# Performance work log

Measured on AMD Instinct MI355X. Metric: run time of the kernel, lower is better.

The kernel has to match this reference:

```python
import jax, jax.numpy as jnp
import numpy as np

S, B, K = 64, 16, 512
QD, KD, A = 512, 512, 256


def setup_inputs() -> dict:
    key = jax.random.key(0)
    ks = jax.random.split(key, 10)
    inv_q = 1.0 / np.sqrt(QD)
    inv_k = 1.0 / np.sqrt(KD)
    inv_a = 1.0 / np.sqrt(A)
    return {
        "queries": jax.random.normal(ks[0], (S, B, QD), dtype=jnp.float32),
        "keys": jax.random.normal(ks[1], (B, K, KD), dtype=jnp.float32),
        "null_mask": jax.random.randint(ks[2], (B, K), 0, 2).astype(jnp.bool_),
        # nn.Linear params (PyTorch layout: weight (out, in), bias (out,))
        "Ww": jax.random.uniform(ks[3], (A, QD), jnp.float32, -inv_q, inv_q),
        "Wb": jax.random.uniform(ks[4], (A,), jnp.float32, -inv_q, inv_q),
        "Uw": jax.random.uniform(ks[5], (A, KD), jnp.float32, -inv_k, inv_k),
        "Ub": jax.random.uniform(ks[6], (A,), jnp.float32, -inv_k, inv_k),
        "vw": jax.random.uniform(ks[7], (1, A), jnp.float32, -inv_a, inv_a),
        "vb": jax.random.uniform(ks[8], (1,), jnp.float32, -inv_a, inv_a),
    }


def reference(queries, keys, null_mask, Ww, Wb, Uw, Ub, vw, vb):
    # t_query: (S, B, A); t_key: (B, K, A)
    t_query = jnp.einsum("sbq,aq->sba", queries, Ww) + Wb
    t_key = jnp.einsum("bkd,ad->bka", keys, Uw) + Ub
    # broadcast add -> (S, B, K, A), tanh, project with v -> alpha (S, B, K)
    h = jnp.tanh(t_query[:, :, None, :] + t_key[None, :, :, :])
    alpha = jnp.einsum("sbka,a->sbk", h, vw[0]) + vb[0]
    alpha = jnp.where(null_mask[None, :, :], -jnp.inf, alpha)
    att_weight = jax.nn.softmax(alpha, axis=2)  # (S, B, K)
    # bmm(att_weight^T, keys)^T -> (S, B, KD)
    attened_keys = jnp.einsum("sbk,bkd->sbd", att_weight, keys)
    return attened_keys, alpha
```

## Files before the change

### kernel.cpp

```cpp
#include <hip/hip_runtime.h>
#include <math.h>

#define S_DIM 64
#define B_DIM 16
#define K_DIM 512
#define QD_DIM 512
#define A_DIM 256

#define NEG_BIG (-3.0e38f)

#define SC 2.8853900817779268f

#define TK_OFF 262144
#define W_WS_OFF ((size_t)2359296)
#define CONV_F32_OFF ((size_t)2883584)
#define CONV_ROWS 9728
#define LO_USHORT_OFF ((size_t)CONV_ROWS * 512)

typedef __attribute__((ext_vector_type(8))) short short8v;
typedef __attribute__((ext_vector_type(4))) float f32x4;

static __device__ __forceinline__ uint2 pack_hi4(float4 v) {
    unsigned x0 = __float_as_uint(v.x), x1 = __float_as_uint(v.y),
             x2 = __float_as_uint(v.z), x3 = __float_as_uint(v.w);
    uint2 r;
    r.x = (x1 & 0xffff0000u) | (x0 >> 16);
    r.y = (x3 & 0xffff0000u) | (x2 >> 16);
    return r;
}
static __device__ __forceinline__ uint2 pack_lo4(float4 v) {
    float l0 = v.x - __uint_as_float(__float_as_uint(v.x) & 0xffff0000u);
    float l1 = v.y - __uint_as_float(__float_as_uint(v.y) & 0xffff0000u);
    float l2 = v.z - __uint_as_float(__float_as_uint(v.z) & 0xffff0000u);
    float l3 = v.w - __uint_as_float(__float_as_uint(v.w) & 0xffff0000u);
    unsigned y0 = __float_as_uint(l0), y1 = __float_as_uint(l1),
             y2 = __float_as_uint(l2), y3 = __float_as_uint(l3);
    uint2 r;
    r.x = (y1 & 0xffff0000u) | (y0 >> 16);
    r.y = (y3 & 0xffff0000u) | (y2 >> 16);
    return r;
}

__global__ __launch_bounds__(256) void conv_kernel(
    const float* __restrict__ q, const float* __restrict__ k,
    const float* __restrict__ ww, const float* __restrict__ uw,
    unsigned short* __restrict__ hi, unsigned short* __restrict__ lo)
{
    const int idx = blockIdx.x * 256 + threadIdx.x;
    const int row = idx >> 6;
    const int c   = (idx & 63) << 3;

    const float* __restrict__ src;
    if (row < 1024)      src = q  + (size_t)row * 512;
    else if (row < 9216) src = k  + (size_t)(row - 1024) * 512;
    else if (row < 9472) src = ww + (size_t)(row - 9216) * 512;
    else                 src = uw + (size_t)(row - 9472) * 512;

    float4 v0 = *(const float4*)(src + c);
    float4 v1 = *(const float4*)(src + c + 4);
    uint2 h0 = pack_hi4(v0), h1 = pack_hi4(v1);
    uint2 l0 = pack_lo4(v0), l1 = pack_lo4(v1);
    uint4 H = {h0.x, h0.y, h1.x, h1.y};
    uint4 L = {l0.x, l0.y, l1.x, l1.y};
    *(uint4*)&hi[(size_t)row * 512 + c] = H;
    *(uint4*)&lo[(size_t)row * 512 + c] = L;
}

__global__ __launch_bounds__(256) void lin_mfma(
    const unsigned short* __restrict__ hi, const unsigned short* __restrict__ lo,
    const float* __restrict__ Wb, const float* __restrict__ Ub,
    float* __restrict__ t_ws)
{
    __shared__ unsigned short Ah[64][40], Al[64][40], Bh[64][40], Bl[64][40];

    const int bx = blockIdx.x;
    const bool isQ = (bx < 64);
    int mt, nt;
    if (isQ) { mt = bx >> 2; nt = bx & 3; }
    else     { int t = bx - 64; mt = t >> 7; nt = t & 127; }

    const int aro = isQ ? (mt * 64) : (9472 + mt * 64);
    const int bro = isQ ? (9216 + nt * 64) : (1024 + nt * 64);

    const int tid  = threadIdx.x;
    const int srow = tid >> 2;
    const int scol = (tid & 3) << 3;
    const int lane = tid & 63, wid = tid >> 6;
    const int wm = (wid >> 1) << 5, wn = (wid & 1) << 5;
    const int fr  = lane & 15;
    const int fkb = (lane >> 4) << 3;

    f32x4 acc[2][2] = {};

    const unsigned short* pAh = hi + (size_t)(aro + srow) * 512 + scol;
    const unsigned short* pAl = lo + (size_t)(aro + srow) * 512 + scol;
    const unsigned short* pBh = hi + (size_t)(bro + srow) * 512 + scol;
    const unsigned short* pBl = lo + (size_t)(bro + srow) * 512 + scol;

    uint4 rah = *(const uint4*)(pAh);
    uint4 ral = *(const uint4*)(pAl);
    uint4 rbh = *(const uint4*)(pBh);
    uint4 rbl = *(const uint4*)(pBl);

    for (int ks = 0; ks < 16; ++ks) {
        __syncthreads();
        *(uint4*)&Ah[srow][scol] = rah;
        *(uint4*)&Al[srow][scol] = ral;
        *(uint4*)&Bh[srow][scol] = rbh;
        *(uint4*)&Bl[srow][scol] = rbl;
        __syncthreads();
        if (ks < 15) {
            const int o = (ks + 1) * 32;
            rah = *(const uint4*)(pAh + o);
            ral = *(const uint4*)(pAl + o);
            rbh = *(const uint4*)(pBh + o);
            rbl = *(const uint4*)(pBl + o);
        }
        short8v bhv[2], blv[2];
        #pragma unroll
        for (int j = 0; j < 2; ++j) {
            bhv[j] = *(const short8v*)&Bh[wn + j * 16 + fr][fkb];
            blv[j] = *(const short8v*)&Bl[wn + j * 16 + fr][fkb];
        }
        #pragma unroll
        for (int i = 0; i < 2; ++i) {
            short8v ah = *(const short8v*)&Ah[wm + i * 16 + fr][fkb];
            short8v al = *(const short8v*)&Al[wm + i * 16 + fr][fkb];
            #pragma unroll
            for (int j = 0; j < 2; ++j) {
                acc[i][j] = __builtin_amdgcn_mfma_f32_16x16x32_bf16(ah, bhv[j], acc[i][j], 0, 0, 0);
                acc[i][j] = __builtin_amdgcn_mfma_f32_16x16x32_bf16(ah, blv[j], acc[i][j], 0, 0, 0);
                acc[i][j] = __builtin_amdgcn_mfma_f32_16x16x32_bf16(al, bhv[j], acc[i][j], 0, 0, 0);
            }
        }
    }

    const int crow = (lane >> 4) << 2;
    if (isQ) {
        #pragma unroll
        for (int j = 0; j < 2; ++j) {
            const int a_col = nt * 64 + wn + j * 16 + fr;
            const float bias = Wb[a_col];
            #pragma unroll
            for (int i = 0; i < 2; ++i)
                #pragma unroll
                for (int r = 0; r < 4; ++r) {
                    const int m = mt * 64 + wm + i * 16 + crow + r;
                    t_ws[(size_t)m * 256 + a_col] =
                        __builtin_amdgcn_exp2f(SC * (acc[i][j][r] + bias));
                }
        }
    } else {
        #pragma unroll
        for (int i = 0; i < 2; ++i)
            #pragma unroll
            for (int r = 0; r < 4; ++r) {
                const int a = mt * 64 + wm + i * 16 + crow + r;
                const float bias = Ub[a];
                #pragma unroll
                for (int j = 0; j < 2; ++j) {
                    const int n = nt * 64 + wn + j * 16 + fr;
                    t_ws[TK_OFF + (size_t)(n >> 9) * 131072 + (size_t)a * 512 + (n & 511)]
                        = __builtin_amdgcn_exp2f(SC * (acc[i][j][r] + bias));
                }
            }
    }
}

__global__ __launch_bounds__(256) void alpha_kernel(
    const float* __restrict__ t_ws, const float* __restrict__ vw,
    const float* __restrict__ vb, const unsigned char* __restrict__ mask,
    float* __restrict__ alpha_out, float* __restrict__ w_ws)
{
    __shared__ float4 pv[256];
    __shared__ float red[5][4];

    const int bid = blockIdx.x;
    const int b  = bid >> 5;
    const int sp = (bid & 31) << 1;
    const int tid = threadIdx.x;
    const int lane = tid & 63, wid = tid >> 6;

    const float myvw = vw[tid];
    {
        float4 p;
        p.x = t_ws[(size_t)(sp * B_DIM + b) * A_DIM + tid];
        p.y = t_ws[(size_t)((sp + 1) * B_DIM + b) * A_DIM + tid];
        p.z = myvw; p.w = 0.f;
        pv[tid] = p;
    }

    float sv = myvw;
    #pragma unroll
    for (int o = 32; o > 0; o >>= 1) sv += __shfl_xor(sv, o);
    if (lane == 0) red[0][wid] = sv;
    __syncthreads();
    const float sumvw = red[0][0] + red[0][1] + red[0][2] + red[0][3];

    const float* __restrict__ ek = t_ws + TK_OFF + (size_t)b * 131072;
    const int k2 = tid * 2;

    float acc00 = 0.f, acc01 = 0.f, acc10 = 0.f, acc11 = 0.f;
    #pragma unroll 4
    for (int a = 0; a < A_DIM; ++a) {
        float2 tv = *(const float2*)&ek[(size_t)a * 512 + k2];
        float4 p = pv[a];
        float r00 = __builtin_amdgcn_rcpf(fmaf(p.x, tv.x, 1.0f));
        float r01 = __builtin_amdgcn_rcpf(fmaf(p.x, tv.y, 1.0f));
        float r10 = __builtin_amdgcn_rcpf(fmaf(p.y, tv.x, 1.0f));
        float r11 = __builtin_amdgcn_rcpf(fmaf(p.y, tv.y, 1.0f));
        acc00 = fmaf(p.z, r00, acc00);
        acc01 = fmaf(p.z, r01, acc01);
        acc10 = fmaf(p.z, r10, acc10);
        acc11 = fmaf(p.z, r11, acc11);
    }

    const float base = sumvw + vb[0];
    float a00 = base - 2.0f * acc00, a01 = base - 2.0f * acc01;
    float a10 = base - 2.0f * acc10, a11 = base - 2.0f * acc11;
    const unsigned char* mrow = mask + b * K_DIM;
    const bool m0 = mrow[k2] != 0, m1 = mrow[k2 + 1] != 0;
    if (m0) { a00 = NEG_BIG; a10 = NEG_BIG; }
    if (m1) { a01 = NEG_BIG; a11 = NEG_BIG; }

    *(float2*)&alpha_out[(size_t)(sp * B_DIM + b) * K_DIM + k2] = make_float2(a00, a01);
    *(float2*)&alpha_out[(size_t)((sp + 1) * B_DIM + b) * K_DIM + k2] = make_float2(a10, a11);

    float mm0 = fmaxf(a00, a01), mm1 = fmaxf(a10, a11);
    #pragma unroll
    for (int o = 32; o > 0; o >>= 1) {
        mm0 = fmaxf(mm0, __shfl_xor(mm0, o));
        mm1 = fmaxf(mm1, __shfl_xor(mm1, o));
    }
    if (lane == 0) { red[1][wid] = mm0; red[2][wid] = mm1; }
    __syncthreads();
    const float mx0 = fmaxf(fmaxf(red[1][0], red[1][1]), fmaxf(red[1][2], red[1][3]));
    const float mx1 = fmaxf(fmaxf(red[2][0], red[2][1]), fmaxf(red[2][2], red[2][3]));

    float e00 = __expf(a00 - mx0), e01 = __expf(a01 - mx0);
    float e10 = __expf(a10 - mx1), e11 = __expf(a11 - mx1);
    float s0 = e00 + e01, s1 = e10 + e11;
    #pragma unroll
    for (int o = 32; o > 0; o >>= 1) {
        s0 += __shfl_xor(s0, o);
        s1 += __shfl_xor(s1, o);
    }
    if (lane == 0) { red[3][wid] = s0; red[4][wid] = s1; }
    __syncthreads();
    const float inv0 = 1.0f / (red[3][0] + red[3][1] + red[3][2] + red[3][3]);
    const float inv1 = 1.0f / (red[4][0] + red[4][1] + red[4][2] + red[4][3]);

    *(float2*)&w_ws[(size_t)(b * S_DIM + sp) * K_DIM + k2] = make_float2(e00 * inv0, e01 * inv0);
    *(float2*)&w_ws[(size_t)(b * S_DIM + sp + 1) * K_DIM + k2] = make_float2(e10 * inv1, e11 * inv1);
}

__global__ __launch_bounds__(256) void att_kernel(
    const float* __restrict__ w_ws, const float* __restrict__ keys,
    float* __restrict__ out_att)
{
    __shared__ float wt[16][68];
    __shared__ float kt[64][64];

    const int d0g = blockIdx.x * 64;
    const int s0  = blockIdx.y * 16;
    const int b   = blockIdx.z;
    const int tid = threadIdx.x;

    const int sL = tid >> 4;
    const int dc = (tid & 15) << 2;

    float acc[4] = {};

    for (int k0 = 0; k0 < K_DIM; k0 += 64) {
        __syncthreads();
        *(float4*)&wt[sL][dc] =
            *(const float4*)&w_ws[(size_t)(b * S_DIM + s0 + sL) * K_DIM + k0 + dc];
        #pragma unroll
        for (int rr = 0; rr < 4; ++rr) {
            const int kr = (tid >> 4) + rr * 16;
            *(float4*)&kt[kr][dc] =
                *(const float4*)&keys[((size_t)b * K_DIM + k0 + kr) * QD_DIM + d0g + dc];
        }
        __syncthreads();
        #pragma unroll
        for (int kk = 0; kk < 64; kk += 4) {
            float4 wv = *(const float4*)&wt[sL][kk];
            float wr[4] = {wv.x, wv.y, wv.z, wv.w};
            #pragma unroll
            for (int u = 0; u < 4; ++u) {
                float4 kv = *(const float4*)&kt[kk + u][dc];
                acc[0] = fmaf(wr[u], kv.x, acc[0]);
                acc[1] = fmaf(wr[u], kv.y, acc[1]);
                acc[2] = fmaf(wr[u], kv.z, acc[2]);
                acc[3] = fmaf(wr[u], kv.w, acc[3]);
            }
        }
    }

    float4 o = {acc[0], acc[1], acc[2], acc[3]};
    *(float4*)&out_att[(size_t)((s0 + sL) * B_DIM + b) * QD_DIM + d0g + dc] = o;
}

extern "C" void kernel_launch(void* const* d_in, const int* in_sizes, int n_in,
                              void* d_out, int out_size, void* d_ws, size_t ws_size,
                              hipStream_t stream) {
    const float* queries = (const float*)d_in[0];
    const float* keys    = (const float*)d_in[1];
    const unsigned char* mask = (const unsigned char*)d_in[2];
    const float* Ww = (const float*)d_in[3];
    const float* Wb = (const float*)d_in[4];
    const float* Uw = (const float*)d_in[5];
    const float* Ub = (const float*)d_in[6];
    const float* vw = (const float*)d_in[7];
    const float* vb = (const float*)d_in[8];

    float* out_att   = (float*)d_out;
    float* out_alpha = (float*)d_out + (size_t)S_DIM * B_DIM * QD_DIM;

    float* t_ws = (float*)d_ws;
    float* w_ws = t_ws + W_WS_OFF;
    unsigned short* hi = (unsigned short*)(t_ws + CONV_F32_OFF);
    unsigned short* lo = hi + LO_USHORT_OFF;

    conv_kernel<<<2432, 256, 0, stream>>>(queries, keys, Ww, Uw, hi, lo);

    lin_mfma<<<576, 256, 0, stream>>>(hi, lo, Wb, Ub, t_ws);

    alpha_kernel<<<512, 256, 0, stream>>>(t_ws, vw, vb, mask,
                                          out_alpha, w_ws);

    dim3 gC(QD_DIM / 64, S_DIM / 16, B_DIM);
    att_kernel<<<gC, 256, 0, stream>>>(w_ws, keys, out_att);
}
```

Before: 145.9 us.

## Split alpha reduction over attention dim into partial sums plus softmax kernel

The alpha kernel's 256-long loop over the attention dimension is split into four chunks computed by separate blocks (2048 blocks instead of 512), which write partial sums to a new workspace region. A separate softmax kernel then sums the partials, applies the mask and computes the softmax per (s,b) row. Separately, the MFMA linear kernel's global-to-register prefetch is deepened from one to two stages. The split raises parallelism on the compute-heavy rcp loop, at the cost of an extra launch and partial-sum traffic through memory.

Measured after the change: 143.4 us. No clear change (-1.7%).

```diff
diff --git a/kernel.cpp b/kernel.cpp
--- a/kernel.cpp
+++ b/kernel.cpp
@@ -13,7 +13,8 @@
 
 #define TK_OFF 262144
 #define W_WS_OFF ((size_t)2359296)
-#define CONV_F32_OFF ((size_t)2883584)
+#define PART_OFF ((size_t)2883584)
+#define CONV_F32_OFF ((size_t)4980736)
 #define CONV_ROWS 9728
 #define LO_USHORT_OFF ((size_t)CONV_ROWS * 512)
 
@@ -97,24 +98,29 @@
     const unsigned short* pBh = hi + (size_t)(bro + srow) * 512 + scol;
     const unsigned short* pBl = lo + (size_t)(bro + srow) * 512 + scol;
 
-    uint4 rah = *(const uint4*)(pAh);
-    uint4 ral = *(const uint4*)(pAl);
-    uint4 rbh = *(const uint4*)(pBh);
-    uint4 rbl = *(const uint4*)(pBl);
+    uint4 c_ah = *(const uint4*)(pAh);
+    uint4 c_al = *(const uint4*)(pAl);
+    uint4 c_bh = *(const uint4*)(pBh);
+    uint4 c_bl = *(const uint4*)(pBl);
+    uint4 n_ah = *(const uint4*)(pAh + 32);
+    uint4 n_al = *(const uint4*)(pAl + 32);
+    uint4 n_bh = *(const uint4*)(pBh + 32);
+    uint4 n_bl = *(const uint4*)(pBl + 32);
 
     for (int ks = 0; ks < 16; ++ks) {
         __syncthreads();
-        *(uint4*)&Ah[srow][scol] = rah;
-        *(uint4*)&Al[srow][scol] = ral;
-        *(uint4*)&Bh[srow][scol] = rbh;
-        *(uint4*)&Bl[srow][scol] = rbl;
+        *(uint4*)&Ah[srow][scol] = c_ah;
+        *(uint4*)&Al[srow][scol] = c_al;
+        *(uint4*)&Bh[srow][scol] = c_bh;
+        *(uint4*)&Bl[srow][scol] = c_bl;
         __syncthreads();
-        if (ks < 15) {
-            const int o = (ks + 1) * 32;
-            rah = *(const uint4*)(pAh + o);
-            ral = *(const uint4*)(pAl + o);
-            rbh = *(const uint4*)(pBh + o);
-            rbl = *(const uint4*)(pBl + o);
+        c_ah = n_ah; c_al = n_al; c_bh = n_bh; c_bl = n_bl;
+        if (ks < 14) {
+            const int o = (ks + 2) * 32;
+            n_ah = *(const uint4*)(pAh + o);
+            n_al = *(const uint4*)(pAl + o);
+            n_bh = *(const uint4*)(pBh + o);
+            n_bl = *(const uint4*)(pBl + o);
         }
         short8v bhv[2], blv[2];
         #pragma unroll
@@ -167,42 +173,37 @@
     }
 }
 
-__global__ __launch_bounds__(256) void alpha_kernel(
+__global__ __launch_bounds__(256) void alpha_part_kernel(
     const float* __restrict__ t_ws, const float* __restrict__ vw,
-    const float* __restrict__ vb, const unsigned char* __restrict__ mask,
-    float* __restrict__ alpha_out, float* __restrict__ w_ws)
-{
-    __shared__ float4 pv[256];
-    __shared__ float red[5][4];
+    float* __restrict__ part)
+{
+    __shared__ float4 pv[64];
 
     const int bid = blockIdx.x;
-    const int b  = bid >> 5;
-    const int sp = (bid & 31) << 1;
+    const int b     = bid >> 7;
+    const int inner = bid & 127;
+    const int ah    = inner >> 5;
+    const int sp    = (inner & 31) << 1;
+    const int a0    = ah << 6;
     const int tid = threadIdx.x;
-    const int lane = tid & 63, wid = tid >> 6;
-
-    const float myvw = vw[tid];
-    {
+
+    if (tid < 64) {
+        const int a = a0 + tid;
         float4 p;
-        p.x = t_ws[(size_t)(sp * B_DIM + b) * A_DIM + tid];
-        p.y = t_ws[(size_t)((sp + 1) * B_DIM + b) * A_DIM + tid];
-        p.z = myvw; p.w = 0.f;
+        p.x = t_ws[(size_t)(sp * B_DIM + b) * A_DIM + a];
+        p.y = t_ws[(size_t)((sp + 1) * B_DIM + b) * A_DIM + a];
+        p.z = vw[a]; p.w = 0.f;
         pv[tid] = p;
     }
-
-    float sv = myvw;
-    #pragma unroll
-    for (int o = 32; o > 0; o >>= 1) sv += __shfl_xor(sv, o);
-    if (lane == 0) red[0][wid] = sv;
     __syncthreads();
-    const float sumvw = red[0][0] + red[0][1] + red[0][2] + red[0][3];
-
-    const float* __restrict__ ek = t_ws + TK_OFF + (size_t)b * 131072;
+
+    const float* __restrict__ ek =
+        t_ws + TK_OFF + (size_t)b * 131072 + (size_t)a0 * 512;
     const int k2 = tid * 2;
 
     float acc00 = 0.f, acc01 = 0.f, acc10 = 0.f, acc11 = 0.f;
     #pragma unroll 4
-    for (int a = 0; a < A_DIM; ++a) {
+    for (int a = 0; a < 64; ++a) {
         float2 tv = *(const float2*)&ek[(size_t)a * 512 + k2];
         float4 p = pv[a];
         float r00 = __builtin_amdgcn_rcpf(fmaf(p.x, tv.x, 1.0f));
@@ -215,43 +216,64 @@
         acc11 = fmaf(p.z, r11, acc11);
     }
 
-    const float base = sumvw + vb[0];
-    float a00 = base - 2.0f * acc00, a01 = base - 2.0f * acc01;
-    float a10 = base - 2.0f * acc10, a11 = base - 2.0f * acc11;
+    const int sb0 = sp * B_DIM + b;
+    float* __restrict__ pp = part + (size_t)ah * 524288;
+    *(float2*)&pp[(size_t)sb0 * 512 + k2]           = make_float2(acc00, acc01);
+    *(float2*)&pp[(size_t)(sb0 + B_DIM) * 512 + k2] = make_float2(acc10, acc11);
+}
+
+__global__ __launch_bounds__(256) void softmax_kernel(
+    const float* __restrict__ part, const float* __restrict__ vw,
+    const float* __restrict__ vb, const unsigned char* __restrict__ mask,
+    float* __restrict__ alpha_out, float* __restrict__ w_ws)
+{
+    __shared__ float red[3][4];
+
+    const int bid = blockIdx.x;
+    const int s = bid >> 4, b = bid & 15;
+    const int sb = s * B_DIM + b;
+    const int tid = threadIdx.x;
+    const int lane = tid & 63, wid = tid >> 6;
+
+    float sv = vw[tid];
+    #pragma unroll
+    for (int o = 32; o > 0; o >>= 1) sv += __shfl_xor(sv, o);
+    if (lane == 0) red[0][wid] = sv;
+    __syncthreads();
+    const float base = red[0][0] + red[0][1] + red[0][2] + red[0][3] + vb[0];
+
+    const int k2 = tid * 2;
+    const size_t po = (size_t)sb * 512 + k2;
+    float2 p0 = *(const float2*)&part[po];
+    float2 p1 = *(const float2*)&part[po + 524288];
+    float2 p2 = *(const float2*)&part[po + 2 * 524288];
+    float2 p3 = *(const float2*)&part[po + 3 * 524288];
+    float a0 = base - 2.0f * (p0.x + p1.x + p2.x + p3.x);
+    float a1 = base - 2.0f * (p0.y + p1.y + p2.y + p3.y);
+
     const unsigned char* mrow = mask + b * K_DIM;
-    const bool m0 = mrow[k2] != 0, m1 = mrow[k2 + 1] != 0;
-    if (m0) { a00 = NEG_BIG; a10 = NEG_BIG; }
-    if (m1) { a01 = NEG_BIG; a11 = NEG_BIG; }
-
-    *(float2*)&alpha_out[(size_t)(sp * B_DIM + b) * K_DIM + k2] = make_float2(a00, a01);
-    *(float2*)&alpha_out[(size_t)((sp + 1) * B_DIM + b) * K_DIM + k2] = make_float2(a10, a11);
-
-    float mm0 = fmaxf(a00, a01), mm1 = fmaxf(a10, a11);
+    if (mrow[k2])     a0 = NEG_BIG;
+    if (mrow[k2 + 1]) a1 = NEG_BIG;
+
+    *(float2*)&alpha_out[(size_t)sb * K_DIM + k2] = make_float2(a0, a1);
+
+    float m = fmaxf(a0, a1);
     #pragma unroll
-    for (int o = 32; o > 0; o >>= 1) {
-        mm0 = fmaxf(mm0, __shfl_xor(mm0, o));
-        mm1 = fmaxf(mm1, __shfl_xor(mm1, o));
-    }
-    if (lane == 0) { red[1][wid] = mm0; red[2][wid] = mm1; }
+    for (int o = 32; o > 0; o >>= 1) m = fmaxf(m, __shfl_xor(m, o));
+    if (lane == 0) red[1][wid] = m;
     __syncthreads();
-    const float mx0 = fmaxf(fmaxf(red[1][0], red[1][1]), fmaxf(red[1][2], red[1][3]));
-    const float mx1 = fmaxf(fmaxf(red[2][0], red[2][1]), fmaxf(red[2][2], red[2][3]));
-
-    float e00 = __expf(a00 - mx0), e01 = __expf(a01 - mx0);
-    float e10 = __expf(a10 - mx1), e11 = __expf(a11 - mx1);
-    float s0 = e00 + e01, s1 = e10 + e11;
+    const float mx = fmaxf(fmaxf(red[1][0], red[1][1]), fmaxf(red[1][2], red[1][3]));
+
+    float e0 = __expf(a0 - mx);
+    float e1 = __expf(a1 - mx);
+    float ssum = e0 + e1;
     #pragma unroll
-    for (int o = 32; o > 0; o >>= 1) {
-        s0 += __shfl_xor(s0, o);
-        s1 += __shfl_xor(s1, o);
-    }
-    if (lane == 0) { red[3][wid] = s0; red[4][wid] = s1; }
+    for (int o = 32; o > 0; o >>= 1) ssum += __shfl_xor(ssum, o);
+    if (lane == 0) red[2][wid] = ssum;
     __syncthreads();
-    const float inv0 = 1.0f / (red[3][0] + red[3][1] + red[3][2] + red[3][3]);
-    const float inv1 = 1.0f / (red[4][0] + red[4][1] + red[4][2] + red[4][3]);
-
-    *(float2*)&w_ws[(size_t)(b * S_DIM + sp) * K_DIM + k2] = make_float2(e00 * inv0, e01 * inv0);
-    *(float2*)&w_ws[(size_t)(b * S_DIM + sp + 1) * K_DIM + k2] = make_float2(e10 * inv1, e11 * inv1);
+    const float inv = 1.0f / (red[2][0] + red[2][1] + red[2][2] + red[2][3]);
+
+    *(float2*)&w_ws[(size_t)(b * S_DIM + s) * K_DIM + k2] = make_float2(e0 * inv, e1 * inv);
 }
 
 __global__ __launch_bounds__(256) void att_kernel(
@@ -319,6 +341,7 @@
 
     float* t_ws = (float*)d_ws;
     float* w_ws = t_ws + W_WS_OFF;
+    float* part = t_ws + PART_OFF;
     unsigned short* hi = (unsigned short*)(t_ws + CONV_F32_OFF);
     unsigned short* lo = hi + LO_USHORT_OFF;
 
@@ -326,8 +349,10 @@
 
     lin_mfma<<<576, 256, 0, stream>>>(hi, lo, Wb, Ub, t_ws);
 
-    alpha_kernel<<<512, 256, 0, stream>>>(t_ws, vw, vb, mask,
-                                          out_alpha, w_ws);
+    alpha_part_kernel<<<2048, 256, 0, stream>>>(t_ws, vw, part);
+
+    softmax_kernel<<<1024, 256, 0, stream>>>(part, vw, vb, mask,
+                                             out_alpha, w_ws);
 
     dim3 gC(QD_DIM / 64, S_DIM / 16, B_DIM);
     att_kernel<<<gC, 256, 0, stream>>>(w_ws, keys, out_att);
```
